# Kernel tuning notes

Hardware: AMD Instinct MI355X
Metric: run time of the kernel (lower is better)

Reference implementation:

```python
import jax, jax.numpy as jnp
import numpy as np

NE = 200000   # num_entities
NR = 16       # num_relations
D  = 128      # embed_dim
B  = 4096     # batch
S  = 64       # neighbors per node
L  = 2        # num_layers
H  = 4        # attention heads (hardcoded in module)


def _ln(x, g, b, eps=1e-5):
    m = jnp.mean(x, -1, keepdims=True)
    v = jnp.mean((x - m) ** 2, -1, keepdims=True)
    return (x - m) * jax.lax.rsqrt(v + eps) * g + b


def setup_inputs() -> dict:
    key = jax.random.key(0)
    ks = jax.random.split(key, 12)
    s = 0.05
    return {
        'drug_entity_indices': jax.random.randint(ks[0], (B,), 0, NE),
        'adj_entity': jax.random.randint(ks[1], (B, S), 0, NE),
        'adj_relation': jax.random.randint(ks[2], (B, S), 0, NR),
        'edge_weights': jax.random.uniform(ks[3], (B, S), dtype=jnp.float32),
        'entity_emb': jax.random.normal(ks[4], (NE, D), jnp.float32) * s,
        'W_rgcn': jax.random.normal(ks[5], (L, NR, D, D), jnp.float32) * s,
        'res_w': jax.random.normal(ks[6], (L, D, D), jnp.float32) * s,
        'res_b': jnp.zeros((L, D), jnp.float32),
        'proj_w': jax.random.normal(ks[7], (L, D, D), jnp.float32) * s,
        'proj_b': jnp.zeros((L, D), jnp.float32),
        'ln_g': jnp.ones((L, D), jnp.float32),
        'ln_b': jnp.zeros((L, D), jnp.float32),
        'in_proj_w': jax.random.normal(ks[8], (3 * D, D), jnp.float32) * s,
        'in_proj_b': jnp.zeros((3 * D,), jnp.float32),
        'out_proj_w': jax.random.normal(ks[9], (D, D), jnp.float32) * s,
        'out_proj_b': jnp.zeros((D,), jnp.float32),
        'fln_g': jnp.ones((D,), jnp.float32),
        'fln_b': jnp.zeros((D,), jnp.float32),
    }


def reference(drug_entity_indices, adj_entity, adj_relation, edge_weights,
              entity_emb, W_rgcn, res_w, res_b, proj_w, proj_b, ln_g, ln_b,
              in_proj_w, in_proj_b, out_proj_w, out_proj_b, fln_g, fln_b):
    node = entity_emb[drug_entity_indices]           # [B,D] combined_emb
    nbr = entity_emb[adj_entity]                     # [B,S,D]
    # Route each edge to its relation: sum_s nbr*ew*[rel==r] then one GEMM per relation
    # (mathematically identical to the per-relation masked matmul loop in torch).
    onehot = jax.nn.one_hot(adj_relation, NR, dtype=node.dtype)      # [B,S,R]
    pre = jnp.einsum('bsd,bsr->brd', nbr * edge_weights[..., None], onehot)
    outs = []
    for l in range(L):
        msgs = jnp.einsum('brd,rde->be', pre, W_rgcn[l])             # [B,D]
        h = jax.nn.relu(node + msgs + node @ res_w[l].T + res_b[l])  # RGCNAggregator
        node = _ln(h @ proj_w[l].T + proj_b[l] + node, ln_g[l], ln_b[l])
        outs.append(node)
    x = jnp.stack(outs, 0)                           # [L,B,D] seq-first
    qkv = x @ in_proj_w.T + in_proj_b
    q, k, v = jnp.split(qkv, 3, axis=-1)
    hd = D // H
    def heads(t):
        return t.reshape(L, B, H, hd).transpose(1, 2, 0, 3)          # [B,H,L,hd]
    q, k, v = heads(q), heads(k), heads(v)
    att = jax.nn.softmax(jnp.einsum('bhld,bhmd->bhlm', q, k) / np.sqrt(hd).astype(np.float32), axis=-1)
    o = jnp.einsum('bhlm,bhmd->bhld', att, v).transpose(2, 0, 1, 3).reshape(L, B, D)
    o = o @ out_proj_w.T + out_proj_b
    return _ln(o.mean(0), fln_g, fln_b)              # [B,D]
```

## Files before the change

kernel.cpp:

```cpp
#include <hip/hip_runtime.h>
#include <math.h>

#define NRREL 16
#define DDIM 128
#define BBATCH 4096
#define SNBR 64

typedef __attribute__((ext_vector_type(8))) short short8;
typedef __attribute__((ext_vector_type(4))) float floatx4;

__device__ __forceinline__ unsigned short f2bf(float f) {
    unsigned u = __builtin_bit_cast(unsigned, f);
    u += 0x7fffu + ((u >> 16) & 1u);
    return (unsigned short)(u >> 16);
}

extern "C" __global__ __launch_bounds__(128)
void k_gather(const int* __restrict__ drug, const int* __restrict__ adj_e,
              const int* __restrict__ adj_r, const float* __restrict__ ew,
              const float* __restrict__ emb,
              unsigned short* __restrict__ pre_bf,
              float* __restrict__ node_f, unsigned short* __restrict__ node_bf)
{
    const int b = blockIdx.x, t = threadIdx.x;
    __shared__ float pre[NRREL * DDIM];
    #pragma unroll
    for (int r = 0; r < NRREL; ++r) pre[r * DDIM + t] = 0.f;
    float nf = emb[(size_t)drug[b] * DDIM + t];
    node_f[(size_t)b * DDIM + t] = nf;
    node_bf[(size_t)b * DDIM + t] = f2bf(nf);
    const int base = b * SNBR;
    #pragma unroll 4
    for (int s = 0; s < SNBR; ++s) {
        int e = adj_e[base + s];
        int r = adj_r[base + s];
        float w = ew[base + s];
        pre[r * DDIM + t] = fmaf(emb[(size_t)e * DDIM + t], w, pre[r * DDIM + t]);
    }
    #pragma unroll
    for (int r = 0; r < NRREL; ++r)
        pre_bf[(size_t)b * 2048 + r * DDIM + t] = f2bf(pre[r * DDIM + t]);
}

extern "C" __global__ __launch_bounds__(256)
void k_wconv(const float* __restrict__ W_rgcn, const float* __restrict__ res_w,
             const float* __restrict__ proj_w, const float* __restrict__ in_w,
             const float* __restrict__ out_w,
             unsigned short* __restrict__ Wcat, unsigned short* __restrict__ resw,
             unsigned short* __restrict__ projw, unsigned short* __restrict__ inw,
             unsigned short* __restrict__ outw)
{
    int i = blockIdx.x * 256 + threadIdx.x;
    if (i < 524288) {
        int n = i >> 11, k = i & 2047;
        int l = n >> 7, e = n & 127;
        Wcat[i] = f2bf(W_rgcn[((size_t)l * 2048 + k) * 128 + e]);
    } else {
        int j = i - 524288;
        if (j < 32768)       resw[j] = f2bf(res_w[j]);
        else if (j < 65536)  projw[j - 32768] = f2bf(proj_w[j - 32768]);
        else if (j < 114688) inw[j - 65536] = f2bf(in_w[j - 65536]);
        else                 outw[j - 114688] = f2bf(out_w[j - 114688]);
    }
}

__device__ __forceinline__ void gemm32x32(const unsigned short* __restrict__ A,
                                          const unsigned short* __restrict__ Bt,
                                          int K, int r0, int c0, floatx4 acc[2][2])
{
    int lane = threadIdx.x & 63;
    int l15 = lane & 15, q = lane >> 4;
    const unsigned short* a0 = A + (size_t)(r0 + l15) * K + q * 8;
    const unsigned short* a1 = a0 + (size_t)16 * K;
    const unsigned short* b0 = Bt + (size_t)(c0 + l15) * K + q * 8;
    const unsigned short* b1 = b0 + (size_t)16 * K;
    #pragma unroll 2
    for (int k = 0; k < K; k += 32) {
        short8 A0 = *(const short8*)(a0 + k);
        short8 A1 = *(const short8*)(a1 + k);
        short8 B0 = *(const short8*)(b0 + k);
        short8 B1 = *(const short8*)(b1 + k);
        acc[0][0] = __builtin_amdgcn_mfma_f32_16x16x32_bf16(A0, B0, acc[0][0], 0, 0, 0);
        acc[0][1] = __builtin_amdgcn_mfma_f32_16x16x32_bf16(A0, B1, acc[0][1], 0, 0, 0);
        acc[1][0] = __builtin_amdgcn_mfma_f32_16x16x32_bf16(A1, B0, acc[1][0], 0, 0, 0);
        acc[1][1] = __builtin_amdgcn_mfma_f32_16x16x32_bf16(A1, B1, acc[1][1], 0, 0, 0);
    }
}

extern "C" __global__ __launch_bounds__(256)
void k_msgs(const unsigned short* __restrict__ pre_bf,
            const unsigned short* __restrict__ Wcat, float* __restrict__ msgs)
{
    int wave = threadIdx.x >> 6, wm = wave >> 1, wn = wave & 1;
    int r0 = blockIdx.x * 64 + wm * 32;
    int c0 = blockIdx.y * 64 + wn * 32;
    floatx4 acc[2][2] = {};
    gemm32x32(pre_bf, Wcat, 2048, r0, c0, acc);
    int lane = threadIdx.x & 63, l15 = lane & 15, q = lane >> 4;
    for (int mi = 0; mi < 2; ++mi)
        for (int ni = 0; ni < 2; ++ni) {
            int gc = c0 + ni * 16 + l15;
            #pragma unroll
            for (int r = 0; r < 4; ++r) {
                int gr = r0 + mi * 16 + 4 * q + r;
                msgs[(size_t)gr * 256 + gc] = acc[mi][ni][r];
            }
        }
}

extern "C" __global__ __launch_bounds__(256)
void k_res(const unsigned short* __restrict__ node_bf, const unsigned short* __restrict__ resw,
           const float* __restrict__ res_b, const float* __restrict__ node_f,
           const float* __restrict__ msgs, unsigned short* __restrict__ h_bf, int l)
{
    int wave = threadIdx.x >> 6, wm = wave >> 1, wn = wave & 1;
    int r0 = blockIdx.x * 64 + wm * 32;
    int c0 = blockIdx.y * 64 + wn * 32;
    floatx4 acc[2][2] = {};
    gemm32x32(node_bf, resw + (size_t)l * DDIM * DDIM, DDIM, r0, c0, acc);
    int lane = threadIdx.x & 63, l15 = lane & 15, q = lane >> 4;
    for (int mi = 0; mi < 2; ++mi)
        for (int ni = 0; ni < 2; ++ni) {
            int gc = c0 + ni * 16 + l15;
            float rb = res_b[l * DDIM + gc];
            #pragma unroll
            for (int r = 0; r < 4; ++r) {
                int gr = r0 + mi * 16 + 4 * q + r;
                float v = acc[mi][ni][r] + rb + node_f[(size_t)gr * DDIM + gc]
                        + msgs[(size_t)gr * 256 + l * DDIM + gc];
                v = v > 0.f ? v : 0.f;
                h_bf[(size_t)gr * DDIM + gc] = f2bf(v);
            }
        }
}

extern "C" __global__ __launch_bounds__(256)
void k_proj(const unsigned short* __restrict__ h_bf, const unsigned short* __restrict__ projw,
            const float* __restrict__ proj_b, const float* __restrict__ ln_g,
            const float* __restrict__ ln_b, float* __restrict__ node_f,
            unsigned short* __restrict__ node_bf, unsigned short* __restrict__ xs_bf, int l)
{
    int wave = threadIdx.x >> 6;
    int r0 = (blockIdx.x * 4 + wave) * 16;
    int lane = threadIdx.x & 63, l15 = lane & 15, q = lane >> 4;
    const unsigned short* Bt = projw + (size_t)l * DDIM * DDIM;
    floatx4 acc[8] = {};
    const unsigned short* ap = h_bf + (size_t)(r0 + l15) * DDIM + q * 8;
    #pragma unroll
    for (int k = 0; k < DDIM; k += 32) {
        short8 A0 = *(const short8*)(ap + k);
        #pragma unroll
        for (int ni = 0; ni < 8; ++ni) {
            short8 B = *(const short8*)(Bt + (size_t)(ni * 16 + l15) * DDIM + q * 8 + k);
            acc[ni] = __builtin_amdgcn_mfma_f32_16x16x32_bf16(A0, B, acc[ni], 0, 0, 0);
        }
    }
    float vv[4][8];
    float s[4] = {0, 0, 0, 0}, sq[4] = {0, 0, 0, 0};
    #pragma unroll
    for (int ni = 0; ni < 8; ++ni) {
        int gc = ni * 16 + l15;
        float pb = proj_b[l * DDIM + gc];
        #pragma unroll
        for (int r = 0; r < 4; ++r) {
            int gr = r0 + 4 * q + r;
            float v = acc[ni][r] + pb + node_f[(size_t)gr * DDIM + gc];
            vv[r][ni] = v; s[r] += v; sq[r] += v * v;
        }
    }
    #pragma unroll
    for (int r = 0; r < 4; ++r)
        #pragma unroll
        for (int off = 8; off >= 1; off >>= 1) {
            s[r] += __shfl_xor(s[r], off, 64);
            sq[r] += __shfl_xor(sq[r], off, 64);
        }
    #pragma unroll
    for (int ni = 0; ni < 8; ++ni) {
        int gc = ni * 16 + l15;
        float g = ln_g[l * DDIM + gc], bb = ln_b[l * DDIM + gc];
        #pragma unroll
        for (int r = 0; r < 4; ++r) {
            int gr = r0 + 4 * q + r;
            float mean = s[r] * (1.f / DDIM);
            float var = sq[r] * (1.f / DDIM) - mean * mean;
            float val = (vv[r][ni] - mean) * rsqrtf(var + 1e-5f) * g + bb;
            node_f[(size_t)gr * DDIM + gc] = val;
            unsigned short vb = f2bf(val);
            node_bf[(size_t)gr * DDIM + gc] = vb;
            xs_bf[(size_t)(2 * gr + l) * DDIM + gc] = vb;
        }
    }
}

extern "C" __global__ __launch_bounds__(256)
void k_qkv(const unsigned short* __restrict__ xs_bf, const unsigned short* __restrict__ inw,
           const float* __restrict__ in_b, float* __restrict__ qkv)
{
    int wave = threadIdx.x >> 6, wm = wave >> 1, wn = wave & 1;
    int r0 = blockIdx.x * 64 + wm * 32;
    int c0 = blockIdx.y * 64 + wn * 32;
    floatx4 acc[2][2] = {};
    gemm32x32(xs_bf, inw, DDIM, r0, c0, acc);
    int lane = threadIdx.x & 63, l15 = lane & 15, q = lane >> 4;
    for (int mi = 0; mi < 2; ++mi)
        for (int ni = 0; ni < 2; ++ni) {
            int gc = c0 + ni * 16 + l15;
            float ib = in_b[gc];
            #pragma unroll
            for (int r = 0; r < 4; ++r) {
                int gr = r0 + mi * 16 + 4 * q + r;
                qkv[(size_t)gr * 384 + gc] = acc[mi][ni][r] + ib;
            }
        }
}

extern "C" __global__ __launch_bounds__(128)
void k_attn(const float* __restrict__ qkv, unsigned short* __restrict__ o_bf)
{
    int b = blockIdx.x, t = threadIdx.x;
    const float* base0 = qkv + (size_t)(2 * b) * 384;
    const float* base1 = base0 + 384;
    float q0 = base0[t], kk0 = base0[128 + t], v0 = base0[256 + t];
    float q1 = base1[t], kk1 = base1[128 + t], v1 = base1[256 + t];
    float s00 = q0 * kk0, s01 = q0 * kk1, s10 = q1 * kk0, s11 = q1 * kk1;
    #pragma unroll
    for (int off = 16; off >= 1; off >>= 1) {
        s00 += __shfl_xor(s00, off, 64);
        s01 += __shfl_xor(s01, off, 64);
        s10 += __shfl_xor(s10, off, 64);
        s11 += __shfl_xor(s11, off, 64);
    }
    const float sc = 0.17677669529663687f;
    s00 *= sc; s01 *= sc; s10 *= sc; s11 *= sc;
    float m0 = fmaxf(s00, s01), e00 = expf(s00 - m0), e01 = expf(s01 - m0);
    float i0 = 1.f / (e00 + e01);
    float m1 = fmaxf(s10, s11), e10 = expf(s10 - m1), e11 = expf(s11 - m1);
    float i1 = 1.f / (e10 + e11);
    o_bf[(size_t)(2 * b) * 128 + t]     = f2bf((e00 * v0 + e01 * v1) * i0);
    o_bf[(size_t)(2 * b + 1) * 128 + t] = f2bf((e10 * v0 + e11 * v1) * i1);
}

extern "C" __global__ __launch_bounds__(256)
void k_out(const unsigned short* __restrict__ o_bf, const unsigned short* __restrict__ outw,
           const float* __restrict__ out_b, const float* __restrict__ fg,
           const float* __restrict__ fb, float* __restrict__ outp)
{
    int wave = threadIdx.x >> 6;
    int r0 = (blockIdx.x * 4 + wave) * 16;
    int lane = threadIdx.x & 63, l15 = lane & 15, q = lane >> 4;
    floatx4 acc[8] = {};
    const unsigned short* ap = o_bf + (size_t)(r0 + l15) * DDIM + q * 8;
    #pragma unroll
    for (int k = 0; k < DDIM; k += 32) {
        short8 A0 = *(const short8*)(ap + k);
        #pragma unroll
        for (int ni = 0; ni < 8; ++ni) {
            short8 B = *(const short8*)(outw + (size_t)(ni * 16 + l15) * DDIM + q * 8 + k);
            acc[ni] = __builtin_amdgcn_mfma_f32_16x16x32_bf16(A0, B, acc[ni], 0, 0, 0);
        }
    }
    float av[2][8];
    float s[2] = {0, 0}, sq[2] = {0, 0};
    #pragma unroll
    for (int ni = 0; ni < 8; ++ni) {
        int gc = ni * 16 + l15;
        float ob = out_b[gc];
        #pragma unroll
        for (int rr = 0; rr < 2; ++rr) {
            float v = 0.5f * (acc[ni][2 * rr] + acc[ni][2 * rr + 1]) + ob;
            av[rr][ni] = v; s[rr] += v; sq[rr] += v * v;
        }
    }
    #pragma unroll
    for (int rr = 0; rr < 2; ++rr)
        #pragma unroll
        for (int off = 8; off >= 1; off >>= 1) {
            s[rr] += __shfl_xor(s[rr], off, 64);
            sq[rr] += __shfl_xor(sq[rr], off, 64);
        }
    #pragma unroll
    for (int ni = 0; ni < 8; ++ni) {
        int gc = ni * 16 + l15;
        float g = fg[gc], bb = fb[gc];
        #pragma unroll
        for (int rr = 0; rr < 2; ++rr) {
            int bg = (r0 >> 1) + 2 * q + rr;
            float mean = s[rr] * (1.f / DDIM);
            float var = sq[rr] * (1.f / DDIM) - mean * mean;
            outp[(size_t)bg * DDIM + gc] = (av[rr][ni] - mean) * rsqrtf(var + 1e-5f) * g + bb;
        }
    }
}

extern "C" void kernel_launch(void* const* d_in, const int* in_sizes, int n_in,
                              void* d_out, int out_size, void* d_ws, size_t ws_size,
                              hipStream_t stream) {
    const int*   drug_idx = (const int*)d_in[0];
    const int*   adj_ent  = (const int*)d_in[1];
    const int*   adj_rel  = (const int*)d_in[2];
    const float* ew       = (const float*)d_in[3];
    const float* emb      = (const float*)d_in[4];
    const float* W_rgcn   = (const float*)d_in[5];
    const float* res_w    = (const float*)d_in[6];
    const float* res_b    = (const float*)d_in[7];
    const float* proj_w   = (const float*)d_in[8];
    const float* proj_b   = (const float*)d_in[9];
    const float* ln_g     = (const float*)d_in[10];
    const float* ln_b     = (const float*)d_in[11];
    const float* in_w     = (const float*)d_in[12];
    const float* in_b     = (const float*)d_in[13];
    const float* out_w    = (const float*)d_in[14];
    const float* out_b    = (const float*)d_in[15];
    const float* fg       = (const float*)d_in[16];
    const float* fb       = (const float*)d_in[17];
    float* outp = (float*)d_out;

    char* ws = (char*)d_ws;
    size_t off = 0;
    auto alloc = [&](size_t bytes) { size_t o = off; off = (off + bytes + 255) & ~(size_t)255; return o; };
    unsigned short* pre_bf  = (unsigned short*)(ws + alloc((size_t)BBATCH * 2048 * 2));
    float*          node_f  = (float*)         (ws + alloc((size_t)BBATCH * 128 * 4));
    unsigned short* node_bf = (unsigned short*)(ws + alloc((size_t)BBATCH * 128 * 2));
    unsigned short* xs_bf   = (unsigned short*)(ws + alloc((size_t)2 * BBATCH * 128 * 2));
    unsigned short* h_bf    = (unsigned short*)(ws + alloc((size_t)BBATCH * 128 * 2));
    float*          msgs    = (float*)         (ws + alloc((size_t)BBATCH * 256 * 4));
    float*          qkv     = (float*)         (ws + alloc((size_t)2 * BBATCH * 384 * 4));
    unsigned short* o_bf    = (unsigned short*)(ws + alloc((size_t)2 * BBATCH * 128 * 2));
    unsigned short* Wcat    = (unsigned short*)(ws + alloc((size_t)256 * 2048 * 2));
    unsigned short* resw    = (unsigned short*)(ws + alloc((size_t)2 * 128 * 128 * 2));
    unsigned short* projw   = (unsigned short*)(ws + alloc((size_t)2 * 128 * 128 * 2));
    unsigned short* inw     = (unsigned short*)(ws + alloc((size_t)384 * 128 * 2));
    unsigned short* outw    = (unsigned short*)(ws + alloc((size_t)128 * 128 * 2));

    hipLaunchKernelGGL(k_wconv, dim3(2560), dim3(256), 0, stream,
                       W_rgcn, res_w, proj_w, in_w, out_w, Wcat, resw, projw, inw, outw);
    hipLaunchKernelGGL(k_gather, dim3(BBATCH), dim3(128), 0, stream,
                       drug_idx, adj_ent, adj_rel, ew, emb, pre_bf, node_f, node_bf);
    hipLaunchKernelGGL(k_msgs, dim3(64, 4), dim3(256), 0, stream, pre_bf, Wcat, msgs);
    for (int l = 0; l < 2; ++l) {
        hipLaunchKernelGGL(k_res, dim3(64, 2), dim3(256), 0, stream,
                           node_bf, resw, res_b, node_f, msgs, h_bf, l);
        hipLaunchKernelGGL(k_proj, dim3(64), dim3(256), 0, stream,
                           h_bf, projw, proj_b, ln_g, ln_b, node_f, node_bf, xs_bf, l);
    }
    hipLaunchKernelGGL(k_qkv, dim3(128, 6), dim3(256), 0, stream, xs_bf, inw, in_b, qkv);
    hipLaunchKernelGGL(k_attn, dim3(BBATCH), dim3(128), 0, stream, qkv, o_bf);
    hipLaunchKernelGGL(k_out, dim3(128), dim3(256), 0, stream, o_bf, outw, out_b, fg, fb, outp);
}
```

Before: 272.9 us.

## Fuse layer and head kernels through LDS, vectorize gather with split accumulators

Fuses the residual GEMM, ReLU and projection+LayerNorm into one per-layer kernel, keeping the hidden tile in LDS. It also fuses the QKV GEMM, two-token attention and output projection+LayerNorm into one head kernel, dropping the h, qkv and o global buffers and several launches. The gather kernel now uses float4 neighbor loads with four wave-group accumulator copies in LDS, summed at the end. The cost is fewer blocks (64 and 128) for the fused kernels and qkv rounded to bf16 before attention, which lowers occupancy and adds precision loss.

```diff
diff --git a/kernel.cpp b/kernel.cpp
--- a/kernel.cpp
+++ b/kernel.cpp
@@ -13,6 +13,9 @@
     unsigned u = __builtin_bit_cast(unsigned, f);
     u += 0x7fffu + ((u >> 16) & 1u);
     return (unsigned short)(u >> 16);
+}
+__device__ __forceinline__ float bf2f(unsigned short u) {
+    return __builtin_bit_cast(float, ((unsigned)u) << 16);
 }
 
 extern "C" __global__ __launch_bounds__(128)
@@ -23,23 +26,39 @@
               float* __restrict__ node_f, unsigned short* __restrict__ node_bf)
 {
     const int b = blockIdx.x, t = threadIdx.x;
-    __shared__ float pre[NRREL * DDIM];
+    const int g = t >> 5, c = t & 31;
+    __shared__ float pre4[4 * NRREL * DDIM];
     #pragma unroll
-    for (int r = 0; r < NRREL; ++r) pre[r * DDIM + t] = 0.f;
-    float nf = emb[(size_t)drug[b] * DDIM + t];
-    node_f[(size_t)b * DDIM + t] = nf;
-    node_bf[(size_t)b * DDIM + t] = f2bf(nf);
+    for (int i = t; i < 4 * NRREL * DDIM; i += 128) pre4[i] = 0.f;
+    __syncthreads();
+
     const int base = b * SNBR;
+    float* myacc = pre4 + g * (NRREL * DDIM) + 4 * c;
     #pragma unroll 4
-    for (int s = 0; s < SNBR; ++s) {
+    for (int i = 0; i < SNBR / 4; ++i) {
+        int s = 4 * i + g;
         int e = adj_e[base + s];
         int r = adj_r[base + s];
         float w = ew[base + s];
-        pre[r * DDIM + t] = fmaf(emb[(size_t)e * DDIM + t], w, pre[r * DDIM + t]);
-    }
+        float4 v = *(const float4*)(emb + (size_t)e * DDIM + 4 * c);
+        float* p = myacc + r * DDIM;
+        p[0] = fmaf(v.x, w, p[0]);
+        p[1] = fmaf(v.y, w, p[1]);
+        p[2] = fmaf(v.z, w, p[2]);
+        p[3] = fmaf(v.w, w, p[3]);
+    }
+    if (t < 32) {
+        float4 nf = *(const float4*)(emb + (size_t)drug[b] * DDIM + 4 * t);
+        *(float4*)(node_f + (size_t)b * DDIM + 4 * t) = nf;
+        ushort4 nb = { f2bf(nf.x), f2bf(nf.y), f2bf(nf.z), f2bf(nf.w) };
+        *(ushort4*)(node_bf + (size_t)b * DDIM + 4 * t) = nb;
+    }
+    __syncthreads();
     #pragma unroll
-    for (int r = 0; r < NRREL; ++r)
-        pre_bf[(size_t)b * 2048 + r * DDIM + t] = f2bf(pre[r * DDIM + t]);
+    for (int idx = t; idx < NRREL * DDIM; idx += 128) {
+        float v = pre4[idx] + pre4[2048 + idx] + pre4[4096 + idx] + pre4[6144 + idx];
+        pre_bf[(size_t)b * 2048 + idx] = f2bf(v);
+    }
 }
 
 extern "C" __global__ __launch_bounds__(256)
@@ -64,18 +83,21 @@
     }
 }
 
-__device__ __forceinline__ void gemm32x32(const unsigned short* __restrict__ A,
-                                          const unsigned short* __restrict__ Bt,
-                                          int K, int r0, int c0, floatx4 acc[2][2])
-{
-    int lane = threadIdx.x & 63;
-    int l15 = lane & 15, q = lane >> 4;
-    const unsigned short* a0 = A + (size_t)(r0 + l15) * K + q * 8;
-    const unsigned short* a1 = a0 + (size_t)16 * K;
-    const unsigned short* b0 = Bt + (size_t)(c0 + l15) * K + q * 8;
-    const unsigned short* b1 = b0 + (size_t)16 * K;
+extern "C" __global__ __launch_bounds__(256)
+void k_msgs(const unsigned short* __restrict__ pre_bf,
+            const unsigned short* __restrict__ Wcat, float* __restrict__ msgs)
+{
+    int wave = threadIdx.x >> 6, wm = wave >> 1, wn = wave & 1;
+    int r0 = blockIdx.x * 64 + wm * 32;
+    int c0 = blockIdx.y * 64 + wn * 32;
+    int lane = threadIdx.x & 63, l15 = lane & 15, q = lane >> 4;
+    floatx4 acc[2][2] = {};
+    const unsigned short* a0 = pre_bf + (size_t)(r0 + l15) * 2048 + q * 8;
+    const unsigned short* a1 = a0 + (size_t)16 * 2048;
+    const unsigned short* b0 = Wcat + (size_t)(c0 + l15) * 2048 + q * 8;
+    const unsigned short* b1 = b0 + (size_t)16 * 2048;
     #pragma unroll 2
-    for (int k = 0; k < K; k += 32) {
+    for (int k = 0; k < 2048; k += 32) {
         short8 A0 = *(const short8*)(a0 + k);
         short8 A1 = *(const short8*)(a1 + k);
         short8 B0 = *(const short8*)(b0 + k);
@@ -85,18 +107,6 @@
         acc[1][0] = __builtin_amdgcn_mfma_f32_16x16x32_bf16(A1, B0, acc[1][0], 0, 0, 0);
         acc[1][1] = __builtin_amdgcn_mfma_f32_16x16x32_bf16(A1, B1, acc[1][1], 0, 0, 0);
     }
-}
-
-extern "C" __global__ __launch_bounds__(256)
-void k_msgs(const unsigned short* __restrict__ pre_bf,
-            const unsigned short* __restrict__ Wcat, float* __restrict__ msgs)
-{
-    int wave = threadIdx.x >> 6, wm = wave >> 1, wn = wave & 1;
-    int r0 = blockIdx.x * 64 + wm * 32;
-    int c0 = blockIdx.y * 64 + wn * 32;
-    floatx4 acc[2][2] = {};
-    gemm32x32(pre_bf, Wcat, 2048, r0, c0, acc);
-    int lane = threadIdx.x & 63, l15 = lane & 15, q = lane >> 4;
     for (int mi = 0; mi < 2; ++mi)
         for (int ni = 0; ni < 2; ++ni) {
             int gc = c0 + ni * 16 + l15;
@@ -109,186 +119,199 @@
 }
 
 extern "C" __global__ __launch_bounds__(256)
-void k_res(const unsigned short* __restrict__ node_bf, const unsigned short* __restrict__ resw,
-           const float* __restrict__ res_b, const float* __restrict__ node_f,
-           const float* __restrict__ msgs, unsigned short* __restrict__ h_bf, int l)
-{
-    int wave = threadIdx.x >> 6, wm = wave >> 1, wn = wave & 1;
-    int r0 = blockIdx.x * 64 + wm * 32;
-    int c0 = blockIdx.y * 64 + wn * 32;
-    floatx4 acc[2][2] = {};
-    gemm32x32(node_bf, resw + (size_t)l * DDIM * DDIM, DDIM, r0, c0, acc);
-    int lane = threadIdx.x & 63, l15 = lane & 15, q = lane >> 4;
-    for (int mi = 0; mi < 2; ++mi)
-        for (int ni = 0; ni < 2; ++ni) {
-            int gc = c0 + ni * 16 + l15;
+void k_layer(const unsigned short* __restrict__ resw, const unsigned short* __restrict__ projw,
+             const float* __restrict__ res_b, const float* __restrict__ proj_b,
+             const float* __restrict__ ln_g, const float* __restrict__ ln_b,
+             const float* __restrict__ msgs,
+             float* __restrict__ node_f, unsigned short* __restrict__ node_bf,
+             unsigned short* __restrict__ xs_bf, int l)
+{
+    __shared__ unsigned short h_lds[64][136];
+    const int t = threadIdx.x, w = t >> 6, lane = t & 63, l15 = lane & 15, q = lane >> 4;
+    const int r0 = blockIdx.x * 64;
+    {
+        const unsigned short* Rw = resw + (size_t)l * DDIM * DDIM;
+        floatx4 acc[8] = {};
+        const unsigned short* ap = node_bf + (size_t)(r0 + 16 * w + l15) * DDIM + 8 * q;
+        #pragma unroll
+        for (int kk = 0; kk < DDIM; kk += 32) {
+            short8 A0 = *(const short8*)(ap + kk);
+            #pragma unroll
+            for (int ni = 0; ni < 8; ++ni) {
+                short8 B = *(const short8*)(Rw + (size_t)(ni * 16 + l15) * DDIM + kk + 8 * q);
+                acc[ni] = __builtin_amdgcn_mfma_f32_16x16x32_bf16(A0, B, acc[ni], 0, 0, 0);
+            }
+        }
+        #pragma unroll
+        for (int ni = 0; ni < 8; ++ni) {
+            int gc = ni * 16 + l15;
             float rb = res_b[l * DDIM + gc];
             #pragma unroll
             for (int r = 0; r < 4; ++r) {
-                int gr = r0 + mi * 16 + 4 * q + r;
-                float v = acc[mi][ni][r] + rb + node_f[(size_t)gr * DDIM + gc]
+                int lr = 16 * w + 4 * q + r, gr = r0 + lr;
+                float v = acc[ni][r] + rb + node_f[(size_t)gr * DDIM + gc]
                         + msgs[(size_t)gr * 256 + l * DDIM + gc];
-                v = v > 0.f ? v : 0.f;
-                h_bf[(size_t)gr * DDIM + gc] = f2bf(v);
-            }
-        }
+                h_lds[lr][gc] = f2bf(v > 0.f ? v : 0.f);
+            }
+        }
+    }
+    __syncthreads();
+    {
+        const unsigned short* Pw = projw + (size_t)l * DDIM * DDIM;
+        floatx4 acc[8] = {};
+        const unsigned short* ap = &h_lds[16 * w + l15][8 * q];
+        #pragma unroll
+        for (int kk = 0; kk < DDIM; kk += 32) {
+            short8 A0 = *(const short8*)(ap + kk);
+            #pragma unroll
+            for (int ni = 0; ni < 8; ++ni) {
+                short8 B = *(const short8*)(Pw + (size_t)(ni * 16 + l15) * DDIM + kk + 8 * q);
+                acc[ni] = __builtin_amdgcn_mfma_f32_16x16x32_bf16(A0, B, acc[ni], 0, 0, 0);
+            }
+        }
+        float vv[4][8];
+        float s[4] = {0, 0, 0, 0}, sq[4] = {0, 0, 0, 0};
+        #pragma unroll
+        for (int ni = 0; ni < 8; ++ni) {
+            int gc = ni * 16 + l15;
+            float pb = proj_b[l * DDIM + gc];
+            #pragma unroll
+            for (int r = 0; r < 4; ++r) {
+                int gr = r0 + 16 * w + 4 * q + r;
+                float v = acc[ni][r] + pb + node_f[(size_t)gr * DDIM + gc];
+                vv[r][ni] = v; s[r] += v; sq[r] += v * v;
+            }
+        }
+        #pragma unroll
+        for (int r = 0; r < 4; ++r)
+            #pragma unroll
+            for (int off = 8; off >= 1; off >>= 1) {
+                s[r] += __shfl_xor(s[r], off, 64);
+                sq[r] += __shfl_xor(sq[r], off, 64);
+            }
+        #pragma unroll
+        for (int ni = 0; ni < 8; ++ni) {
+            int gc = ni * 16 + l15;
+            float g = ln_g[l * DDIM + gc], bb = ln_b[l * DDIM + gc];
+            #pragma unroll
+            for (int r = 0; r < 4; ++r) {
+                int gr = r0 + 16 * w + 4 * q + r;
+                float mean = s[r] * (1.f / DDIM);
+                float var = sq[r] * (1.f / DDIM) - mean * mean;
+                float val = (vv[r][ni] - mean) * rsqrtf(var + 1e-5f) * g + bb;
+                node_f[(size_t)gr * DDIM + gc] = val;
+                unsigned short vb = f2bf(val);
+                node_bf[(size_t)gr * DDIM + gc] = vb;
+                xs_bf[(size_t)(2 * gr + l) * DDIM + gc] = vb;
+            }
+        }
+    }
 }
 
 extern "C" __global__ __launch_bounds__(256)
-void k_proj(const unsigned short* __restrict__ h_bf, const unsigned short* __restrict__ projw,
-            const float* __restrict__ proj_b, const float* __restrict__ ln_g,
-            const float* __restrict__ ln_b, float* __restrict__ node_f,
-            unsigned short* __restrict__ node_bf, unsigned short* __restrict__ xs_bf, int l)
-{
-    int wave = threadIdx.x >> 6;
-    int r0 = (blockIdx.x * 4 + wave) * 16;
-    int lane = threadIdx.x & 63, l15 = lane & 15, q = lane >> 4;
-    const unsigned short* Bt = projw + (size_t)l * DDIM * DDIM;
-    floatx4 acc[8] = {};
-    const unsigned short* ap = h_bf + (size_t)(r0 + l15) * DDIM + q * 8;
-    #pragma unroll
-    for (int k = 0; k < DDIM; k += 32) {
-        short8 A0 = *(const short8*)(ap + k);
-        #pragma unroll
-        for (int ni = 0; ni < 8; ++ni) {
-            short8 B = *(const short8*)(Bt + (size_t)(ni * 16 + l15) * DDIM + q * 8 + k);
-            acc[ni] = __builtin_amdgcn_mfma_f32_16x16x32_bf16(A0, B, acc[ni], 0, 0, 0);
-        }
-    }
-    float vv[4][8];
-    float s[4] = {0, 0, 0, 0}, sq[4] = {0, 0, 0, 0};
-    #pragma unroll
-    for (int ni = 0; ni < 8; ++ni) {
-        int gc = ni * 16 + l15;
-        float pb = proj_b[l * DDIM + gc];
-        #pragma unroll
-        for (int r = 0; r < 4; ++r) {
-            int gr = r0 + 4 * q + r;
-            float v = acc[ni][r] + pb + node_f[(size_t)gr * DDIM + gc];
-            vv[r][ni] = v; s[r] += v; sq[r] += v * v;
-        }
-    }
-    #pragma unroll
-    for (int r = 0; r < 4; ++r)
-        #pragma unroll
-        for (int off = 8; off >= 1; off >>= 1) {
-            s[r] += __shfl_xor(s[r], off, 64);
-            sq[r] += __shfl_xor(sq[r], off, 64);
-        }
-    #pragma unroll
-    for (int ni = 0; ni < 8; ++ni) {
-        int gc = ni * 16 + l15;
-        float g = ln_g[l * DDIM + gc], bb = ln_b[l * DDIM + gc];
-        #pragma unroll
-        for (int r = 0; r < 4; ++r) {
-            int gr = r0 + 4 * q + r;
-            float mean = s[r] * (1.f / DDIM);
-            float var = sq[r] * (1.f / DDIM) - mean * mean;
-            float val = (vv[r][ni] - mean) * rsqrtf(var + 1e-5f) * g + bb;
-            node_f[(size_t)gr * DDIM + gc] = val;
-            unsigned short vb = f2bf(val);
-            node_bf[(size_t)gr * DDIM + gc] = vb;
-            xs_bf[(size_t)(2 * gr + l) * DDIM + gc] = vb;
-        }
-    }
-}
-
-extern "C" __global__ __launch_bounds__(256)
-void k_qkv(const unsigned short* __restrict__ xs_bf, const unsigned short* __restrict__ inw,
-           const float* __restrict__ in_b, float* __restrict__ qkv)
-{
-    int wave = threadIdx.x >> 6, wm = wave >> 1, wn = wave & 1;
-    int r0 = blockIdx.x * 64 + wm * 32;
-    int c0 = blockIdx.y * 64 + wn * 32;
-    floatx4 acc[2][2] = {};
-    gemm32x32(xs_bf, inw, DDIM, r0, c0, acc);
-    int lane = threadIdx.x & 63, l15 = lane & 15, q = lane >> 4;
-    for (int mi = 0; mi < 2; ++mi)
-        for (int ni = 0; ni < 2; ++ni) {
-            int gc = c0 + ni * 16 + l15;
+void k_head(const unsigned short* __restrict__ xs_bf, const unsigned short* __restrict__ inw,
+            const float* __restrict__ in_b, const unsigned short* __restrict__ outw,
+            const float* __restrict__ out_b, const float* __restrict__ fg,
+            const float* __restrict__ fb, float* __restrict__ outp)
+{
+    __shared__ unsigned short qkv_lds[64][392];
+    __shared__ unsigned short o_lds[64][136];
+    const int t = threadIdx.x, w = t >> 6, lane = t & 63, l15 = lane & 15, q = lane >> 4;
+    const int r0 = blockIdx.x * 64;
+    {
+        floatx4 acc[24] = {};
+        const unsigned short* ap = xs_bf + (size_t)(r0 + 16 * w + l15) * DDIM + 8 * q;
+        #pragma unroll
+        for (int kk = 0; kk < DDIM; kk += 32) {
+            short8 A0 = *(const short8*)(ap + kk);
+            #pragma unroll
+            for (int ni = 0; ni < 24; ++ni) {
+                short8 B = *(const short8*)(inw + (size_t)(ni * 16 + l15) * DDIM + kk + 8 * q);
+                acc[ni] = __builtin_amdgcn_mfma_f32_16x16x32_bf16(A0, B, acc[ni], 0, 0, 0);
+            }
+        }
+        #pragma unroll
+        for (int ni = 0; ni < 24; ++ni) {
+            int gc = ni * 16 + l15;
             float ib = in_b[gc];
             #pragma unroll
-            for (int r = 0; r < 4; ++r) {
-                int gr = r0 + mi * 16 + 4 * q + r;
-                qkv[(size_t)gr * 384 + gc] = acc[mi][ni][r] + ib;
-            }
-        }
-}
-
-extern "C" __global__ __launch_bounds__(128)
-void k_attn(const float* __restrict__ qkv, unsigned short* __restrict__ o_bf)
-{
-    int b = blockIdx.x, t = threadIdx.x;
-    const float* base0 = qkv + (size_t)(2 * b) * 384;
-    const float* base1 = base0 + 384;
-    float q0 = base0[t], kk0 = base0[128 + t], v0 = base0[256 + t];
-    float q1 = base1[t], kk1 = base1[128 + t], v1 = base1[256 + t];
-    float s00 = q0 * kk0, s01 = q0 * kk1, s10 = q1 * kk0, s11 = q1 * kk1;
-    #pragma unroll
-    for (int off = 16; off >= 1; off >>= 1) {
-        s00 += __shfl_xor(s00, off, 64);
-        s01 += __shfl_xor(s01, off, 64);
-        s10 += __shfl_xor(s10, off, 64);
-        s11 += __shfl_xor(s11, off, 64);
-    }
-    const float sc = 0.17677669529663687f;
-    s00 *= sc; s01 *= sc; s10 *= sc; s11 *= sc;
-    float m0 = fmaxf(s00, s01), e00 = expf(s00 - m0), e01 = expf(s01 - m0);
-    float i0 = 1.f / (e00 + e01);
-    float m1 = fmaxf(s10, s11), e10 = expf(s10 - m1), e11 = expf(s11 - m1);
-    float i1 = 1.f / (e10 + e11);
-    o_bf[(size_t)(2 * b) * 128 + t]     = f2bf((e00 * v0 + e01 * v1) * i0);
-    o_bf[(size_t)(2 * b + 1) * 128 + t] = f2bf((e10 * v0 + e11 * v1) * i1);
-}
-
-extern "C" __global__ __launch_bounds__(256)
-void k_out(const unsigned short* __restrict__ o_bf, const unsigned short* __restrict__ outw,
-           const float* __restrict__ out_b, const float* __restrict__ fg,
-           const float* __restrict__ fb, float* __restrict__ outp)
-{
-    int wave = threadIdx.x >> 6;
-    int r0 = (blockIdx.x * 4 + wave) * 16;
-    int lane = threadIdx.x & 63, l15 = lane & 15, q = lane >> 4;
-    floatx4 acc[8] = {};
-    const unsigned short* ap = o_bf + (size_t)(r0 + l15) * DDIM + q * 8;
-    #pragma unroll
-    for (int k = 0; k < DDIM; k += 32) {
-        short8 A0 = *(const short8*)(ap + k);
-        #pragma unroll
-        for (int ni = 0; ni < 8; ++ni) {
-            short8 B = *(const short8*)(outw + (size_t)(ni * 16 + l15) * DDIM + q * 8 + k);
-            acc[ni] = __builtin_amdgcn_mfma_f32_16x16x32_bf16(A0, B, acc[ni], 0, 0, 0);
-        }
-    }
-    float av[2][8];
-    float s[2] = {0, 0}, sq[2] = {0, 0};
-    #pragma unroll
-    for (int ni = 0; ni < 8; ++ni) {
-        int gc = ni * 16 + l15;
-        float ob = out_b[gc];
-        #pragma unroll
-        for (int rr = 0; rr < 2; ++rr) {
-            float v = 0.5f * (acc[ni][2 * rr] + acc[ni][2 * rr + 1]) + ob;
-            av[rr][ni] = v; s[rr] += v; sq[rr] += v * v;
-        }
-    }
-    #pragma unroll
-    for (int rr = 0; rr < 2; ++rr)
-        #pragma unroll
-        for (int off = 8; off >= 1; off >>= 1) {
-            s[rr] += __shfl_xor(s[rr], off, 64);
-            sq[rr] += __shfl_xor(sq[rr], off, 64);
-        }
-    #pragma unroll
-    for (int ni = 0; ni < 8; ++ni) {
-        int gc = ni * 16 + l15;
-        float g = fg[gc], bb = fb[gc];
-        #pragma unroll
-        for (int rr = 0; rr < 2; ++rr) {
-            int bg = (r0 >> 1) + 2 * q + rr;
-            float mean = s[rr] * (1.f / DDIM);
-            float var = sq[rr] * (1.f / DDIM) - mean * mean;
-            outp[(size_t)bg * DDIM + gc] = (av[rr][ni] - mean) * rsqrtf(var + 1e-5f) * g + bb;
+            for (int r = 0; r < 4; ++r)
+                qkv_lds[16 * w + 4 * q + r][gc] = f2bf(acc[ni][r] + ib);
+        }
+    }
+    __syncthreads();
+    {
+        int g = t >> 3, j = t & 7;
+        const unsigned short* row0 = qkv_lds[2 * g];
+        const unsigned short* row1 = qkv_lds[2 * g + 1];
+        float p00 = 0.f, p01 = 0.f, p10 = 0.f, p11 = 0.f;
+        #pragma unroll
+        for (int dd = 0; dd < 16; ++dd) {
+            int d = 16 * j + dd;
+            float q0 = bf2f(row0[d]), k0 = bf2f(row0[128 + d]);
+            float q1 = bf2f(row1[d]), k1 = bf2f(row1[128 + d]);
+            p00 = fmaf(q0, k0, p00); p01 = fmaf(q0, k1, p01);
+            p10 = fmaf(q1, k0, p10); p11 = fmaf(q1, k1, p11);
+        }
+        p00 += __shfl_xor(p00, 1, 64); p01 += __shfl_xor(p01, 1, 64);
+        p10 += __shfl_xor(p10, 1, 64); p11 += __shfl_xor(p11, 1, 64);
+        const float sc = 0.17677669529663687f;
+        p00 *= sc; p01 *= sc; p10 *= sc; p11 *= sc;
+        float m0 = fmaxf(p00, p01), e00 = expf(p00 - m0), e01 = expf(p01 - m0);
+        float i0 = 1.f / (e00 + e01);
+        float m1 = fmaxf(p10, p11), e10 = expf(p10 - m1), e11 = expf(p11 - m1);
+        float i1 = 1.f / (e10 + e11);
+        #pragma unroll
+        for (int dd = 0; dd < 16; ++dd) {
+            int d = 16 * j + dd;
+            float v0 = bf2f(row0[256 + d]), v1 = bf2f(row1[256 + d]);
+            o_lds[2 * g][d]     = f2bf((e00 * v0 + e01 * v1) * i0);
+            o_lds[2 * g + 1][d] = f2bf((e10 * v0 + e11 * v1) * i1);
+        }
+    }
+    __syncthreads();
+    {
+        floatx4 acc[8] = {};
+        const unsigned short* ap = &o_lds[16 * w + l15][8 * q];
+        #pragma unroll
+        for (int kk = 0; kk < DDIM; kk += 32) {
+            short8 A0 = *(const short8*)(ap + kk);
+            #pragma unroll
+            for (int ni = 0; ni < 8; ++ni) {
+                short8 B = *(const short8*)(outw + (size_t)(ni * 16 + l15) * DDIM + kk + 8 * q);
+                acc[ni] = __builtin_amdgcn_mfma_f32_16x16x32_bf16(A0, B, acc[ni], 0, 0, 0);
+            }
+        }
+        float av[2][8];
+        float s[2] = {0, 0}, sq[2] = {0, 0};
+        #pragma unroll
+        for (int ni = 0; ni < 8; ++ni) {
+            int gc = ni * 16 + l15;
+            float ob = out_b[gc];
+            #pragma unroll
+            for (int rr = 0; rr < 2; ++rr) {
+                float v = 0.5f * (acc[ni][2 * rr] + acc[ni][2 * rr + 1]) + ob;
+                av[rr][ni] = v; s[rr] += v; sq[rr] += v * v;
+            }
+        }
+        #pragma unroll
+        for (int rr = 0; rr < 2; ++rr)
+            #pragma unroll
+            for (int off = 8; off >= 1; off >>= 1) {
+                s[rr] += __shfl_xor(s[rr], off, 64);
+                sq[rr] += __shfl_xor(sq[rr], off, 64);
+            }
+        #pragma unroll
+        for (int ni = 0; ni < 8; ++ni) {
+            int gc = ni * 16 + l15;
+            float g = fg[gc], bb = fb[gc];
+            #pragma unroll
+            for (int rr = 0; rr < 2; ++rr) {
+                int bg = blockIdx.x * 32 + 8 * w + 2 * q + rr;
+                float mean = s[rr] * (1.f / DDIM);
+                float var = sq[rr] * (1.f / DDIM) - mean * mean;
+                outp[(size_t)bg * DDIM + gc] = (av[rr][ni] - mean) * rsqrtf(var + 1e-5f) * g + bb;
+            }
         }
     }
 }
@@ -323,10 +346,7 @@
     float*          node_f  = (float*)         (ws + alloc((size_t)BBATCH * 128 * 4));
     unsigned short* node_bf = (unsigned short*)(ws + alloc((size_t)BBATCH * 128 * 2));
     unsigned short* xs_bf   = (unsigned short*)(ws + alloc((size_t)2 * BBATCH * 128 * 2));
-    unsigned short* h_bf    = (unsigned short*)(ws + alloc((size_t)BBATCH * 128 * 2));
     float*          msgs    = (float*)         (ws + alloc((size_t)BBATCH * 256 * 4));
-    float*          qkv     = (float*)         (ws + alloc((size_t)2 * BBATCH * 384 * 4));
-    unsigned short* o_bf    = (unsigned short*)(ws + alloc((size_t)2 * BBATCH * 128 * 2));
     unsigned short* Wcat    = (unsigned short*)(ws + alloc((size_t)256 * 2048 * 2));
     unsigned short* resw    = (unsigned short*)(ws + alloc((size_t)2 * 128 * 128 * 2));
     unsigned short* projw   = (unsigned short*)(ws + alloc((size_t)2 * 128 * 128 * 2));
@@ -338,13 +358,10 @@
     hipLaunchKernelGGL(k_gather, dim3(BBATCH), dim3(128), 0, stream,
                        drug_idx, adj_ent, adj_rel, ew, emb, pre_bf, node_f, node_bf);
     hipLaunchKernelGGL(k_msgs, dim3(64, 4), dim3(256), 0, stream, pre_bf, Wcat, msgs);
-    for (int l = 0; l < 2; ++l) {
-        hipLaunchKernelGGL(k_res, dim3(64, 2), dim3(256), 0, stream,
-                           node_bf, resw, res_b, node_f, msgs, h_bf, l);
-        hipLaunchKernelGGL(k_proj, dim3(64), dim3(256), 0, stream,
-                           h_bf, projw, proj_b, ln_g, ln_b, node_f, node_bf, xs_bf, l);
-    }
-    hipLaunchKernelGGL(k_qkv, dim3(128, 6), dim3(256), 0, stream, xs_bf, inw, in_b, qkv);
-    hipLaunchKernelGGL(k_attn, dim3(BBATCH), dim3(128), 0, stream, qkv, o_bf);
-    hipLaunchKernelGGL(k_out, dim3(128), dim3(256), 0, stream, o_bf, outw, out_b, fg, fb, outp);
-}
+    for (int l = 0; l < 2; ++l)
+        hipLaunchKernelGGL(k_layer, dim3(64), dim3(256), 0, stream,
+                           resw, projw, res_b, proj_b, ln_g, ln_b, msgs,
+                           node_f, node_bf, xs_bf, l);
+    hipLaunchKernelGGL(k_head, dim3(128), dim3(256), 0, stream,
+                       xs_bf, inw, in_b, outw, out_b, fg, fb, outp);
+}
```

New measurement: 279.3 us. +2.3%, slower.
